# Kernel tuning notes

Measured on AMD Instinct MI355X. Metric: run time of the kernel, lower is better.

## Reference

```python
import jax, jax.numpy as jnp
import numpy as np

B, L, Q = 1024, 200, 1
DQ, DF = 512, 128
H, D1, D2 = 4, 128, 64


def setup_inputs() -> dict:
    key = jax.random.key(0)
    ks = jax.random.split(key, 20)
    inp = {
        "query": jax.random.normal(ks[0], (B, Q, DQ), jnp.float32),
        "fact": jax.random.normal(ks[1], (B, L, DF), jnp.float32),
        "mask": jax.random.randint(ks[2], (B, L), 0, 2, jnp.int32),
        "mm_cosine": jax.random.normal(ks[3], (2, B, L), jnp.float32),
    }
    # per-head FCRepeat weights, init per reset_parameters: randn/sqrt(fan_in), bias 0.1
    def w(k, fan_in, fan_out):
        return jax.random.normal(k, (H, fan_in, fan_out), jnp.float32) / np.sqrt(fan_in).astype(np.float32)
    inp["Wq1"] = w(ks[4], DQ, D1); inp["bq1"] = jnp.full((H, D1), 0.1, jnp.float32)
    inp["Wq2"] = w(ks[5], D1, D2); inp["bq2"] = jnp.full((H, D2), 0.1, jnp.float32)
    inp["Wf1"] = w(ks[6], DF, D1); inp["bf1"] = jnp.full((H, D1), 0.1, jnp.float32)
    inp["Wf2"] = w(ks[7], D1, D2); inp["bf2"] = jnp.full((H, D2), 0.1, jnp.float32)
    inp["Wv1"] = w(ks[8], DF, D1); inp["bv1"] = jnp.full((H, D1), 0.1, jnp.float32)
    inp["Wv2"] = w(ks[9], D1, D2); inp["bv2"] = jnp.full((H, D2), 0.1, jnp.float32)
    inp["tau1"] = jnp.full((2, H), 0.1, jnp.float32)   # cosine_tau1
    inp["tau2"] = jnp.full((3, H), 1.0, jnp.float32)   # cosine_tau2
    return inp


def _silu(x):
    return x * jax.nn.sigmoid(x)


def reference(query, fact, mask, mm_cosine,
              Wq1, bq1, Wq2, bq2, Wf1, bf1, Wf2, bf2, Wv1, bv1, Wv2, bv2,
              tau1, tau2):
    # per-head FC stacks (identity acts inside FCRepeat), then SiLU gating
    fq = jnp.einsum('bqi,hio->hbqo', query, Wq1) + bq1[:, None, None, :]
    fq = jnp.einsum('hbqi,hio->hbqo', fq, Wq2) + bq2[:, None, None, :]
    fq = _silu(fq)                                   # [H,B,1,D2]
    ff = jnp.einsum('bli,hio->hblo', fact, Wf1) + bf1[:, None, None, :]
    ff = jnp.einsum('hbli,hio->hblo', ff, Wf2) + bf2[:, None, None, :]
    ff = _silu(ff)                                   # [H,B,L,D2]
    fv = jnp.einsum('bli,hio->hblo', fact, Wv1) + bv1[:, None, None, :]
    fv = jnp.einsum('hbli,hio->hblo', fv, Wv2) + bv2[:, None, None, :]
    fv = _silu(fv)                                   # [H,B,L,D2]

    dot = jnp.einsum('hbld,hbqd->hblq', ff, fq)      # [H,B,L,1]
    dot = dot + (-1e9) * (1.0 - mask.astype(jnp.float32))[None, :, :, None]

    # cosine-bias cross terms
    bias = (mm_cosine[0][None] / tau1[0][:, None, None]
            + mm_cosine[1][None] / tau1[1][:, None, None])[..., None]  # [H,B,L,1]
    b1, b2, b3 = (tau2[i][:, None, None, None] for i in range(3))
    dot = b1 * dot + b2 * bias + b3 * dot * bias

    alphas = jax.nn.softmax(dot, axis=2) + 1e-7      # softmax over L
    out = jnp.einsum('hbld,hblq->hbdq', fv, alphas)[..., 0]  # [H,B,D2]
    return jnp.transpose(out, (1, 0, 2)).reshape(out.shape[1], -1)  # [B,H*D2]
```

## Files before the change

kernel.cpp:

```cpp
#include <hip/hip_runtime.h>
#include <hip/hip_bf16.h>

typedef __attribute__((ext_vector_type(8))) short short8;
typedef __attribute__((ext_vector_type(4))) float f32x4;

#define NH   4
#define NB   1024
#define NL   200
#define NDQ  512
#define NDF  128
#define ND1  128
#define ND2  64
#define KP   128
#define NW   13
#define NT   (NW*64)
#define HIMG (3*ND2*KP*2)
#define SGRAN (3*ND2*16)

#define OFF_WQC   0
#define OFF_BQC   (NH*NDQ*ND2*4)
#define OFF_FQ    (OFF_BQC + NH*ND2*4)
#define OFF_WIMG  (OFF_FQ + NH*NB*ND2*4)
#define OFF_BFC   (OFF_WIMG + NH*HIMG)
#define OFF_BVC   (OFF_BFC + NH*ND2*4)

#define GLOAD_LDS16(gp, lp) __builtin_amdgcn_global_load_lds(                 \
    (const __attribute__((address_space(1))) void*)(gp),                      \
    (__attribute__((address_space(3))) void*)(lp), 16, 0, 0)

__device__ inline short f2bf(float f) {
    union { float f; unsigned u; } v; v.f = f;
    unsigned r = (v.u + 0x7FFFu + ((v.u >> 16) & 1u)) >> 16;
    return (short)r;
}
__device__ inline float bf2f(short s) {
    union { unsigned u; float f; } v; v.u = ((unsigned)(unsigned short)s) << 16;
    return v.f;
}
__device__ inline float fsilu(float z) {
    return z * __fdividef(1.f, 1.f + __expf(-z));
}

template<int CTRL>
__device__ inline float dppf(float x) {
    return __int_as_float(__builtin_amdgcn_update_dpp(0, __float_as_int(x), CTRL, 0xF, 0xF, true));
}
__device__ inline float red16_add(float s) {
    s += dppf<0xB1>(s);
    s += dppf<0x4E>(s);
    s += dppf<0x141>(s);
    s += dppf<0x140>(s);
    return s;
}
__device__ inline float swap16_add(float x) {
    auto p = __builtin_amdgcn_permlane16_swap(__float_as_uint(x), __float_as_uint(x), false, false);
    return __uint_as_float(p[0]) + __uint_as_float(p[1]);
}
__device__ inline float swap32_add(float x) {
    auto p = __builtin_amdgcn_permlane32_swap(__float_as_uint(x), __float_as_uint(x), false, false);
    return __uint_as_float(p[0]) + __uint_as_float(p[1]);
}
__device__ inline float swap16_max(float x) {
    auto p = __builtin_amdgcn_permlane16_swap(__float_as_uint(x), __float_as_uint(x), false, false);
    return fmaxf(__uint_as_float(p[0]), __uint_as_float(p[1]));
}
__device__ inline float swap32_max(float x) {
    auto p = __builtin_amdgcn_permlane32_swap(__float_as_uint(x), __float_as_uint(x), false, false);
    return fmaxf(__uint_as_float(p[0]), __uint_as_float(p[1]));
}

__global__ __launch_bounds__(256) void k_combine(
    const float* __restrict__ Wq1, const float* __restrict__ bq1,
    const float* __restrict__ Wq2, const float* __restrict__ bq2,
    const float* __restrict__ Wf1, const float* __restrict__ bf1,
    const float* __restrict__ Wf2, const float* __restrict__ bf2,
    const float* __restrict__ Wv1, const float* __restrict__ bv1,
    const float* __restrict__ Wv2, const float* __restrict__ bv2,
    float* __restrict__ WQC, float* __restrict__ BQC,
    __hip_bfloat16* __restrict__ WIMG, float* __restrict__ BFC, float* __restrict__ BVC)
{
    int g = blockIdx.x * 256 + threadIdx.x;
    if (g < NH*NDQ*ND2) {
        int h = g >> 15, r = g & 32767, i = r >> 6, j = r & 63;
        const float* a  = Wq1 + (h*NDQ + i)*ND1;
        const float* bb = Wq2 + h*ND1*ND2 + j;
        float s = 0.f;
        for (int k = 0; k < ND1; ++k) s += a[k] * bb[k*ND2];
        WQC[(h*NDQ + i)*ND2 + j] = s;
        return;
    }
    g -= NH*NDQ*ND2;
    if (g < 2*NH*NDF*ND2) {
        int which = (g >= NH*NDF*ND2);
        int r0 = g & (NH*NDF*ND2 - 1);
        int h = r0 >> 13, r = r0 & 8191, i = r >> 6, j = r & 63;
        const float* W1 = (which ? Wv1 : Wf1) + (h*NDF + i)*ND1;
        const float* W2 = (which ? Wv2 : Wf2) + h*ND1*ND2 + j;
        float s = 0.f;
        for (int k = 0; k < ND1; ++k) s += W1[k] * W2[k*ND2];
        short hi = f2bf(s);
        short lo = f2bf(s - bf2f(hi));
        __hip_bfloat16* img = WIMG + (size_t)((h*3 + (which ? 2 : 0))*ND2 + j)*KP + i;
        ((short*)img)[0] = hi;
        if (!which) ((short*)img)[ND2*KP] = lo;
        return;
    }
    g -= 2*NH*NDF*ND2;
    if (g < NH*ND2) {
        int h = g >> 6, j = g & 63;
        float s = bq2[h*ND2 + j];
        for (int k = 0; k < ND1; ++k) s += bq1[h*ND1 + k] * Wq2[(h*ND1 + k)*ND2 + j];
        BQC[g] = s; return;
    }
    g -= NH*ND2;
    if (g < NH*ND2) {
        int h = g >> 6, j = g & 63;
        float s = bf2[h*ND2 + j];
        for (int k = 0; k < ND1; ++k) s += bf1[h*ND1 + k] * Wf2[(h*ND1 + k)*ND2 + j];
        BFC[g] = s; return;
    }
    g -= NH*ND2;
    if (g < NH*ND2) {
        int h = g >> 6, j = g & 63;
        float s = bv2[h*ND2 + j];
        for (int k = 0; k < ND1; ++k) s += bv1[h*ND1 + k] * Wv2[(h*ND1 + k)*ND2 + j];
        BVC[g] = s; return;
    }
}

__global__ __launch_bounds__(256) void k_fq(
    const float* __restrict__ query, const float* __restrict__ WQC,
    const float* __restrict__ BQC, float* __restrict__ FQ)
{
    __shared__ __align__(16) float qS[2*NDQ];
    const int t = threadIdx.x;
    const int b0 = blockIdx.x * 2;
    {
        const float4* src = (const float4*)(query + (size_t)b0 * NDQ);
        ((float4*)qS)[t] = src[t];
    }
    __syncthreads();
    const int h = t >> 6, d = t & 63;
    float s0, s1;
    s0 = s1 = BQC[h*ND2 + d];
    const float* wp = WQC + (size_t)h*NDQ*ND2 + d;
    #pragma unroll 16
    for (int i = 0; i < NDQ; ++i) {
        float wv = wp[i*ND2];
        s0 += qS[i]       * wv;
        s1 += qS[NDQ + i] * wv;
    }
    float* o = FQ + ((size_t)h*NB + b0)*ND2 + d;
    o[0]   = fsilu(s0);
    o[ND2] = fsilu(s1);
}

__global__ __launch_bounds__(NT) __attribute__((amdgpu_waves_per_eu(4, 4))) void k_main(
    const float* __restrict__ fact,
    const int* __restrict__ mask,
    const float* __restrict__ mmc,
    const float* __restrict__ tau1,
    const float* __restrict__ tau2,
    const float* __restrict__ FQ,
    const float* __restrict__ BFC,
    const float* __restrict__ BVC,
    const __hip_bfloat16* __restrict__ WIMG,
    float* __restrict__ out)
{
    __shared__ __align__(16) __hip_bfloat16 wS[2][3*ND2*KP];
    __shared__ __align__(16) float pS[2][NW][132];
    __shared__ __align__(16) float fqS[NH][ND2];
    __shared__ __align__(16) float bfcS[NH][ND2];
    __shared__ __align__(16) float bvcS[NH][ND2];

    const int t    = threadIdx.x;
    const int b    = blockIdx.x;
    const int w    = t >> 6;
    const int lane = t & 63;
    const int a15  = lane & 15;
    const int quad = lane >> 4;
    const int qrot = quad + 2*(a15 & 7);

    const int bL = b * NL;

    auto DMA = [&](int hh) {
        const char* hb = (const char*)WIMG + (size_t)hh*HIMG;
        char* lb = (char*)&wS[hh & 1][0];
        #pragma unroll
        for (int j = 0; j < 4; ++j) {
            int c = w*4 + j;
            if (c < SGRAN/64) {
                int i = c*64 + lane;
                int row = i >> 4;
                int g = ((i & 15) - 2*(row & 7)) & 15;
                GLOAD_LDS16(hb + (row*16 + g)*16, lb + c*1024);
            }
        }
    };

    DMA(0);

    float cval = 0.f;
    if (t < 256)       cval = FQ[(((size_t)(t >> 6))*NB + b)*ND2 + (t & 63)];
    else if (t < 512)  cval = BFC[t - 256];
    else if (t < 768)  cval = BVC[t - 512];
    float mkv[4], c0v[4], c1v[4];
    {
        int rbase = w*16 + quad*4;
        for (int rg = 0; rg < 4; ++rg) {
            int r = rbase + rg;
            if (r < NL) {
                mkv[rg] = 1e9f * (1.0f - (float)mask[bL + r]);
                c0v[rg] = mmc[bL + r];
                c1v[rg] = mmc[NB*NL + bL + r];
            } else { mkv[rg] = 0.f; c0v[rg] = 0.f; c1v[rg] = 0.f; }
        }
    }

    short8 afh[4], afl[4];
    const short8 zero8 = {0,0,0,0,0,0,0,0};
    {
        int row = w*16 + a15;
        for (int kk = 0; kk < 4; ++kk) {
            short8 vh = zero8, vl = zero8;
            if (row < NL) {
                const float* p = fact + ((size_t)(bL + row))*NDF + kk*32 + quad*8;
                float4 x0 = *(const float4*)p;
                float4 x1 = *(const float4*)(p + 4);
                float v[8] = {x0.x, x0.y, x0.z, x0.w, x1.x, x1.y, x1.z, x1.w};
                for (int j = 0; j < 8; ++j) {
                    short hs = f2bf(v[j]);
                    vh[j] = hs;
                    vl[j] = f2bf(v[j] - bf2f(hs));
                }
            }
            afh[kk] = vh;
            afl[kk] = vl;
        }
    }

    if (t < 256)       ((float*)fqS)[t]        = cval;
    else if (t < 512)  ((float*)bfcS)[t - 256] = cval;
    else if (t < 768)  ((float*)bvcS)[t - 512] = cval;
    __syncthreads();

    const f32x4 zf = {0.f, 0.f, 0.f, 0.f};

    auto GEMMS = [&](f32x4 (&aF)[4], f32x4 (&aV)[4], const __hip_bfloat16* wb) {
        #pragma unroll
        for (int nt = 0; nt < 4; ++nt) { aF[nt] = zf; aV[nt] = zf; }
        #pragma unroll
        for (int kk = 0; kk < 4; ++kk) {
            const int gk = ((kk*4 + qrot) & 15) << 3;
            short8 bh[4], bl[4];
            #pragma unroll
            for (int nt = 0; nt < 4; ++nt) {
                const __hip_bfloat16* p = wb + (nt*16 + a15)*KP + gk;
                bh[nt] = *(const short8*)p;
                bl[nt] = *(const short8*)(p + ND2*KP);
            }
            #pragma unroll
            for (int nt = 0; nt < 4; ++nt) {
                aF[nt] = __builtin_amdgcn_mfma_f32_16x16x32_bf16(afh[kk], bh[nt], aF[nt], 0, 0, 0);
                aF[nt] = __builtin_amdgcn_mfma_f32_16x16x32_bf16(afh[kk], bl[nt], aF[nt], 0, 0, 0);
                aF[nt] = __builtin_amdgcn_mfma_f32_16x16x32_bf16(afl[kk], bh[nt], aF[nt], 0, 0, 0);
            }
        }
        #pragma unroll
        for (int kk = 0; kk < 4; ++kk) {
            const int gk = ((kk*4 + qrot) & 15) << 3;
            short8 bv[4];
            #pragma unroll
            for (int nt = 0; nt < 4; ++nt)
                bv[nt] = *(const short8*)(wb + (2*ND2 + nt*16 + a15)*KP + gk);
            #pragma unroll
            for (int nt = 0; nt < 4; ++nt)
                aV[nt] = __builtin_amdgcn_mfma_f32_16x16x32_bf16(afh[kk], bv[nt], aV[nt], 0, 0, 0);
        }
    };

    auto FINISH = [&](f32x4 (&aF)[4], f32x4 (&aV)[4], int h) {
        const float rt1a = __fdividef(1.f, tau1[h]);
        const float rt1b = __fdividef(1.f, tau1[NH + h]);
        const float t20 = tau2[h];
        const float t21 = tau2[NH + h];
        const float t22 = tau2[2*NH + h];
        float fqv[4], bfcv[4], bvcv[4];
        #pragma unroll
        for (int nt = 0; nt < 4; ++nt) {
            fqv[nt]  = fqS[h][nt*16 + a15];
            bfcv[nt] = bfcS[h][nt*16 + a15];
            bvcv[nt] = bvcS[h][nt*16 + a15];
        }
        float lg[4];
        #pragma unroll
        for (int rg = 0; rg < 4; ++rg) {
            float l = -3.0e38f;
            float s = 0.f;
            #pragma unroll
            for (int nt = 0; nt < 4; ++nt)
                s += fsilu(aF[nt][rg] + bfcv[nt]) * fqv[nt];
            s = red16_add(s);
            int r = w*16 + quad*4 + rg;
            if (r < NL) {
                float dv = s - mkv[rg];
                float bias = c0v[rg]*rt1a + c1v[rg]*rt1b;
                l = t20*dv + t21*bias + t22*dv*bias;
            }
            lg[rg] = l;
        }
        float m = fmaxf(fmaxf(lg[0], lg[1]), fmaxf(lg[2], lg[3]));
        m = swap32_max(swap16_max(m));
        float sw = 0.f;
        #pragma unroll
        for (int rg = 0; rg < 4; ++rg) {
            float p = __expf(lg[rg] - m);
            lg[rg] = p;
            sw += p;
        }
        sw = swap32_add(swap16_add(sw));
        float oE[4] = {0.f,0.f,0.f,0.f}, oS[4] = {0.f,0.f,0.f,0.f};
        #pragma unroll
        for (int rg = 0; rg < 4; ++rg) {
            float p = lg[rg];
            int r = w*16 + quad*4 + rg;
            float vm = (r < NL) ? 1.f : 0.f;
            #pragma unroll
            for (int nt = 0; nt < 4; ++nt) {
                float sv = fsilu(aV[nt][rg] + bvcv[nt]);
                oE[nt] += p * sv;
                oS[nt] += vm * sv;
            }
        }
        #pragma unroll
        for (int nt = 0; nt < 4; ++nt) {
            oE[nt] = swap32_add(swap16_add(oE[nt]));
            oS[nt] = swap32_add(swap16_add(oS[nt]));
        }
        if (lane == 0) { pS[h & 1][w][0] = m; pS[h & 1][w][1] = sw; }
        if (quad == 0)
            #pragma unroll
            for (int nt = 0; nt < 4; ++nt) {
                pS[h & 1][w][2  + nt*16 + a15] = oE[nt];
                pS[h & 1][w][66 + nt*16 + a15] = oS[nt];
            }
    };

    auto MERGE = [&](int hm) {
        const int ps = hm & 1;
        float M = pS[ps][0][0];
        for (int ww = 1; ww < NW; ++ww) M = fmaxf(M, pS[ps][ww][0]);
        float den = 0.f, num = 0.f, s1 = 0.f;
        for (int ww = 0; ww < NW; ++ww) {
            float e = __expf(pS[ps][ww][0] - M);
            den += e * pS[ps][ww][1];
            num += e * pS[ps][ww][2 + lane];
            s1  += pS[ps][ww][66 + lane];
        }
        out[(size_t)b*(NH*ND2) + hm*ND2 + lane] = num * __fdividef(1.f, den) + 1e-7f * s1;
    };

    f32x4 aFA[4], aVA[4], aFB[4], aVB[4];

    DMA(1);
    GEMMS(aFA, aVA, &wS[0][0]);
    __syncthreads();

    DMA(2);
    GEMMS(aFB, aVB, &wS[1][0]);
    FINISH(aFA, aVA, 0);
    __syncthreads();

    DMA(3);
    if (w == 9) MERGE(0);
    GEMMS(aFA, aVA, &wS[0][0]);
    FINISH(aFB, aVB, 1);
    __syncthreads();

    if (w == 10) MERGE(1);
    GEMMS(aFB, aVB, &wS[1][0]);
    FINISH(aFA, aVA, 2);
    __syncthreads();

    if (w == 11) MERGE(2);
    FINISH(aFB, aVB, 3);
    __syncthreads();

    if (w == 12) MERGE(3);
}

extern "C" void kernel_launch(void* const* d_in, const int* in_sizes, int n_in,
                              void* d_out, int out_size, void* d_ws, size_t ws_size,
                              hipStream_t stream) {
    const float* query = (const float*)d_in[0];
    const float* fact  = (const float*)d_in[1];
    const int*   maskp = (const int*)d_in[2];
    const float* mmc   = (const float*)d_in[3];
    const float* Wq1 = (const float*)d_in[4];
    const float* bq1 = (const float*)d_in[5];
    const float* Wq2 = (const float*)d_in[6];
    const float* bq2 = (const float*)d_in[7];
    const float* Wf1 = (const float*)d_in[8];
    const float* bf1 = (const float*)d_in[9];
    const float* Wf2 = (const float*)d_in[10];
    const float* bf2 = (const float*)d_in[11];
    const float* Wv1 = (const float*)d_in[12];
    const float* bv1 = (const float*)d_in[13];
    const float* Wv2 = (const float*)d_in[14];
    const float* bv2 = (const float*)d_in[15];
    const float* tau1 = (const float*)d_in[16];
    const float* tau2 = (const float*)d_in[17];

    char* ws = (char*)d_ws;
    float*          WQC  = (float*)(ws + OFF_WQC);
    float*          BQC  = (float*)(ws + OFF_BQC);
    float*          FQ   = (float*)(ws + OFF_FQ);
    __hip_bfloat16* WIMG = (__hip_bfloat16*)(ws + OFF_WIMG);
    float*          BFC  = (float*)(ws + OFF_BFC);
    float*          BVC  = (float*)(ws + OFF_BVC);

    k_combine<<<771, 256, 0, stream>>>(Wq1, bq1, Wq2, bq2, Wf1, bf1, Wf2, bf2,
                                       Wv1, bv1, Wv2, bv2, WQC, BQC, WIMG, BFC, BVC);
    k_fq<<<NB/2, 256, 0, stream>>>(query, WQC, BQC, FQ);
    k_main<<<NB, NT, 0, stream>>>(fact, maskp, mmc, tau1, tau2, FQ, BFC, BVC, WIMG,
                                  (float*)d_out);
}
```

Measured before the change: 384.4 us.

## Split each batch row across two 8-wave blocks and merge partials in a separate kernel

```diff
diff --git a/kernel.cpp b/kernel.cpp
--- a/kernel.cpp
+++ b/kernel.cpp
@@ -12,8 +12,8 @@
 #define ND1  128
 #define ND2  64
 #define KP   128
-#define NW   13
-#define NT   (NW*64)
+#define NWB  8
+#define NTB  (NWB*64)
 #define HIMG (3*ND2*KP*2)
 #define SGRAN (3*ND2*16)
 
@@ -23,6 +23,7 @@
 #define OFF_WIMG  (OFF_FQ + NH*NB*ND2*4)
 #define OFF_BFC   (OFF_WIMG + NH*HIMG)
 #define OFF_BVC   (OFF_BFC + NH*ND2*4)
+#define OFF_PART  (OFF_BVC + NH*ND2*4)
 
 #define GLOAD_LDS16(gp, lp) __builtin_amdgcn_global_load_lds(                 \
     (const __attribute__((address_space(1))) void*)(gp),                      \
@@ -155,7 +156,7 @@
     o[ND2] = fsilu(s1);
 }
 
-__global__ __launch_bounds__(NT) __attribute__((amdgpu_waves_per_eu(4, 4))) void k_main(
+__global__ __launch_bounds__(NTB) void k_main(
     const float* __restrict__ fact,
     const int* __restrict__ mask,
     const float* __restrict__ mmc,
@@ -165,51 +166,51 @@
     const float* __restrict__ BFC,
     const float* __restrict__ BVC,
     const __hip_bfloat16* __restrict__ WIMG,
-    float* __restrict__ out)
+    float* __restrict__ gws)
 {
-    __shared__ __align__(16) __hip_bfloat16 wS[2][3*ND2*KP];
-    __shared__ __align__(16) float pS[2][NW][132];
+    __shared__ __align__(16) __hip_bfloat16 wS[3*ND2*KP];
+    __shared__ __align__(16) float pS[2][NWB][132];
     __shared__ __align__(16) float fqS[NH][ND2];
     __shared__ __align__(16) float bfcS[NH][ND2];
     __shared__ __align__(16) float bvcS[NH][ND2];
 
     const int t    = threadIdx.x;
-    const int b    = blockIdx.x;
+    const int blk  = blockIdx.x;
+    const int b    = blk >> 1;
+    const int half = blk & 1;
     const int w    = t >> 6;
     const int lane = t & 63;
     const int a15  = lane & 15;
     const int quad = lane >> 4;
     const int qrot = quad + 2*(a15 & 7);
 
+    const int tile = half ? (7 + w) : w;
+    const bool act = half ? (w < 6) : (w < 7);
     const int bL = b * NL;
 
     auto DMA = [&](int hh) {
         const char* hb = (const char*)WIMG + (size_t)hh*HIMG;
-        char* lb = (char*)&wS[hh & 1][0];
         #pragma unroll
-        for (int j = 0; j < 4; ++j) {
-            int c = w*4 + j;
-            if (c < SGRAN/64) {
-                int i = c*64 + lane;
-                int row = i >> 4;
-                int g = ((i & 15) - 2*(row & 7)) & 15;
-                GLOAD_LDS16(hb + (row*16 + g)*16, lb + c*1024);
-            }
+        for (int j = 0; j < 6; ++j) {
+            int c = w*6 + j;
+            int i = c*64 + lane;
+            int row = i >> 4;
+            int g = ((i & 15) - 2*(row & 7)) & 15;
+            GLOAD_LDS16(hb + (row*16 + g)*16, (char*)wS + c*1024);
         }
     };
 
     DMA(0);
 
-    float cval = 0.f;
-    if (t < 256)       cval = FQ[(((size_t)(t >> 6))*NB + b)*ND2 + (t & 63)];
-    else if (t < 512)  cval = BFC[t - 256];
-    else if (t < 768)  cval = BVC[t - 512];
+    float cval = 0.f, cval2 = 0.f;
+    if (t < 256) { cval = FQ[(((size_t)(t >> 6))*NB + b)*ND2 + (t & 63)]; cval2 = BVC[t]; }
+    else         { cval = BFC[t - 256]; }
     float mkv[4], c0v[4], c1v[4];
     {
-        int rbase = w*16 + quad*4;
+        int rbase = tile*16 + quad*4;
         for (int rg = 0; rg < 4; ++rg) {
             int r = rbase + rg;
-            if (r < NL) {
+            if (act && r < NL) {
                 mkv[rg] = 1e9f * (1.0f - (float)mask[bL + r]);
                 c0v[rg] = mmc[bL + r];
                 c1v[rg] = mmc[NB*NL + bL + r];
@@ -220,10 +221,10 @@
     short8 afh[4], afl[4];
     const short8 zero8 = {0,0,0,0,0,0,0,0};
     {
-        int row = w*16 + a15;
+        int row = tile*16 + a15;
         for (int kk = 0; kk < 4; ++kk) {
             short8 vh = zero8, vl = zero8;
-            if (row < NL) {
+            if (act && row < NL) {
                 const float* p = fact + ((size_t)(bL + row))*NDF + kk*32 + quad*8;
                 float4 x0 = *(const float4*)p;
                 float4 x1 = *(const float4*)(p + 4);
@@ -239,154 +240,156 @@
         }
     }
 
-    if (t < 256)       ((float*)fqS)[t]        = cval;
-    else if (t < 512)  ((float*)bfcS)[t - 256] = cval;
-    else if (t < 768)  ((float*)bvcS)[t - 512] = cval;
+    if (t < 256) { ((float*)fqS)[t] = cval; ((float*)bvcS)[t] = cval2; }
+    else         { ((float*)bfcS)[t - 256] = cval; }
     __syncthreads();
 
     const f32x4 zf = {0.f, 0.f, 0.f, 0.f};
 
-    auto GEMMS = [&](f32x4 (&aF)[4], f32x4 (&aV)[4], const __hip_bfloat16* wb) {
-        #pragma unroll
-        for (int nt = 0; nt < 4; ++nt) { aF[nt] = zf; aV[nt] = zf; }
-        #pragma unroll
-        for (int kk = 0; kk < 4; ++kk) {
-            const int gk = ((kk*4 + qrot) & 15) << 3;
-            short8 bh[4], bl[4];
+    for (int h = 0; h < NH; ++h) {
+        if (act) {
+            const float rt1a = __fdividef(1.f, tau1[h]);
+            const float rt1b = __fdividef(1.f, tau1[NH + h]);
+            const float t20 = tau2[h];
+            const float t21 = tau2[NH + h];
+            const float t22 = tau2[2*NH + h];
+            float fqv[4], bfcv[4], bvcv[4];
             #pragma unroll
             for (int nt = 0; nt < 4; ++nt) {
-                const __hip_bfloat16* p = wb + (nt*16 + a15)*KP + gk;
-                bh[nt] = *(const short8*)p;
-                bl[nt] = *(const short8*)(p + ND2*KP);
+                fqv[nt]  = fqS[h][nt*16 + a15];
+                bfcv[nt] = bfcS[h][nt*16 + a15];
+                bvcv[nt] = bvcS[h][nt*16 + a15];
+            }
+
+            f32x4 acc[4];
+            #pragma unroll
+            for (int nt = 0; nt < 4; ++nt) acc[nt] = zf;
+            #pragma unroll
+            for (int kk = 0; kk < 4; ++kk) {
+                const int gk = ((kk*4 + qrot) & 15) << 3;
+                short8 bh[4], bl[4];
+                #pragma unroll
+                for (int nt = 0; nt < 4; ++nt) {
+                    const __hip_bfloat16* p = wS + (nt*16 + a15)*KP + gk;
+                    bh[nt] = *(const short8*)p;
+                    bl[nt] = *(const short8*)(p + ND2*KP);
+                }
+                #pragma unroll
+                for (int nt = 0; nt < 4; ++nt) {
+                    acc[nt] = __builtin_amdgcn_mfma_f32_16x16x32_bf16(afh[kk], bh[nt], acc[nt], 0, 0, 0);
+                    acc[nt] = __builtin_amdgcn_mfma_f32_16x16x32_bf16(afh[kk], bl[nt], acc[nt], 0, 0, 0);
+                    acc[nt] = __builtin_amdgcn_mfma_f32_16x16x32_bf16(afl[kk], bh[nt], acc[nt], 0, 0, 0);
+                }
+            }
+
+            float lg[4];
+            #pragma unroll
+            for (int rg = 0; rg < 4; ++rg) {
+                float l = -3.0e38f;
+                float s = 0.f;
+                #pragma unroll
+                for (int nt = 0; nt < 4; ++nt)
+                    s += fsilu(acc[nt][rg] + bfcv[nt]) * fqv[nt];
+                s = red16_add(s);
+                int r = tile*16 + quad*4 + rg;
+                if (r < NL) {
+                    float dv = s - mkv[rg];
+                    float bias = c0v[rg]*rt1a + c1v[rg]*rt1b;
+                    l = t20*dv + t21*bias + t22*dv*bias;
+                }
+                lg[rg] = l;
+            }
+
+            float m = fmaxf(fmaxf(lg[0], lg[1]), fmaxf(lg[2], lg[3]));
+            m = swap32_max(swap16_max(m));
+            float sw = 0.f;
+            #pragma unroll
+            for (int rg = 0; rg < 4; ++rg) {
+                float p = __expf(lg[rg] - m);
+                lg[rg] = p;
+                sw += p;
+            }
+            sw = swap32_add(swap16_add(sw));
+
+            #pragma unroll
+            for (int nt = 0; nt < 4; ++nt) acc[nt] = zf;
+            #pragma unroll
+            for (int kk = 0; kk < 4; ++kk) {
+                const int gk = ((kk*4 + qrot) & 15) << 3;
+                short8 bv[4];
+                #pragma unroll
+                for (int nt = 0; nt < 4; ++nt)
+                    bv[nt] = *(const short8*)(wS + (2*ND2 + nt*16 + a15)*KP + gk);
+                #pragma unroll
+                for (int nt = 0; nt < 4; ++nt)
+                    acc[nt] = __builtin_amdgcn_mfma_f32_16x16x32_bf16(afh[kk], bv[nt], acc[nt], 0, 0, 0);
+            }
+
+            float oE[4] = {0.f,0.f,0.f,0.f}, oS[4] = {0.f,0.f,0.f,0.f};
+            #pragma unroll
+            for (int rg = 0; rg < 4; ++rg) {
+                float p = lg[rg];
+                int r = tile*16 + quad*4 + rg;
+                float vm = (r < NL) ? 1.f : 0.f;
+                #pragma unroll
+                for (int nt = 0; nt < 4; ++nt) {
+                    float sv = fsilu(acc[nt][rg] + bvcv[nt]);
+                    oE[nt] += p * sv;
+                    oS[nt] += vm * sv;
+                }
             }
             #pragma unroll
             for (int nt = 0; nt < 4; ++nt) {
-                aF[nt] = __builtin_amdgcn_mfma_f32_16x16x32_bf16(afh[kk], bh[nt], aF[nt], 0, 0, 0);
-                aF[nt] = __builtin_amdgcn_mfma_f32_16x16x32_bf16(afh[kk], bl[nt], aF[nt], 0, 0, 0);
-                aF[nt] = __builtin_amdgcn_mfma_f32_16x16x32_bf16(afl[kk], bh[nt], aF[nt], 0, 0, 0);
-            }
+                oE[nt] = swap32_add(swap16_add(oE[nt]));
+                oS[nt] = swap32_add(swap16_add(oS[nt]));
+            }
+            if (lane == 0) { pS[h & 1][w][0] = m; pS[h & 1][w][1] = sw; }
+            if (quad == 0)
+                #pragma unroll
+                for (int nt = 0; nt < 4; ++nt) {
+                    pS[h & 1][w][2  + nt*16 + a15] = oE[nt];
+                    pS[h & 1][w][66 + nt*16 + a15] = oS[nt];
+                }
         }
-        #pragma unroll
-        for (int kk = 0; kk < 4; ++kk) {
-            const int gk = ((kk*4 + qrot) & 15) << 3;
-            short8 bv[4];
-            #pragma unroll
-            for (int nt = 0; nt < 4; ++nt)
-                bv[nt] = *(const short8*)(wb + (2*ND2 + nt*16 + a15)*KP + gk);
-            #pragma unroll
-            for (int nt = 0; nt < 4; ++nt)
-                aV[nt] = __builtin_amdgcn_mfma_f32_16x16x32_bf16(afh[kk], bv[nt], aV[nt], 0, 0, 0);
+        __syncthreads();
+
+        if (h + 1 < NH) DMA(h + 1);
+
+        if (w == 7) {
+            const int ps = h & 1;
+            const int nAct = half ? 6 : 7;
+            float M = pS[ps][0][0];
+            for (int ww = 1; ww < nAct; ++ww) M = fmaxf(M, pS[ps][ww][0]);
+            float den = 0.f, num = 0.f, s1 = 0.f;
+            for (int ww = 0; ww < nAct; ++ww) {
+                float e = __expf(pS[ps][ww][0] - M);
+                den += e * pS[ps][ww][1];
+                num += e * pS[ps][ww][2 + lane];
+                s1  += pS[ps][ww][66 + lane];
+            }
+            float* gp = gws + (((size_t)b*2 + half)*NH + h)*132;
+            if (lane == 0) { gp[0] = M; gp[1] = den; }
+            gp[2 + lane]  = num;
+            gp[66 + lane] = s1;
         }
-    };
-
-    auto FINISH = [&](f32x4 (&aF)[4], f32x4 (&aV)[4], int h) {
-        const float rt1a = __fdividef(1.f, tau1[h]);
-        const float rt1b = __fdividef(1.f, tau1[NH + h]);
-        const float t20 = tau2[h];
-        const float t21 = tau2[NH + h];
-        const float t22 = tau2[2*NH + h];
-        float fqv[4], bfcv[4], bvcv[4];
-        #pragma unroll
-        for (int nt = 0; nt < 4; ++nt) {
-            fqv[nt]  = fqS[h][nt*16 + a15];
-            bfcv[nt] = bfcS[h][nt*16 + a15];
-            bvcv[nt] = bvcS[h][nt*16 + a15];
-        }
-        float lg[4];
-        #pragma unroll
-        for (int rg = 0; rg < 4; ++rg) {
-            float l = -3.0e38f;
-            float s = 0.f;
-            #pragma unroll
-            for (int nt = 0; nt < 4; ++nt)
-                s += fsilu(aF[nt][rg] + bfcv[nt]) * fqv[nt];
-            s = red16_add(s);
-            int r = w*16 + quad*4 + rg;
-            if (r < NL) {
-                float dv = s - mkv[rg];
-                float bias = c0v[rg]*rt1a + c1v[rg]*rt1b;
-                l = t20*dv + t21*bias + t22*dv*bias;
-            }
-            lg[rg] = l;
-        }
-        float m = fmaxf(fmaxf(lg[0], lg[1]), fmaxf(lg[2], lg[3]));
-        m = swap32_max(swap16_max(m));
-        float sw = 0.f;
-        #pragma unroll
-        for (int rg = 0; rg < 4; ++rg) {
-            float p = __expf(lg[rg] - m);
-            lg[rg] = p;
-            sw += p;
-        }
-        sw = swap32_add(swap16_add(sw));
-        float oE[4] = {0.f,0.f,0.f,0.f}, oS[4] = {0.f,0.f,0.f,0.f};
-        #pragma unroll
-        for (int rg = 0; rg < 4; ++rg) {
-            float p = lg[rg];
-            int r = w*16 + quad*4 + rg;
-            float vm = (r < NL) ? 1.f : 0.f;
-            #pragma unroll
-            for (int nt = 0; nt < 4; ++nt) {
-                float sv = fsilu(aV[nt][rg] + bvcv[nt]);
-                oE[nt] += p * sv;
-                oS[nt] += vm * sv;
-            }
-        }
-        #pragma unroll
-        for (int nt = 0; nt < 4; ++nt) {
-            oE[nt] = swap32_add(swap16_add(oE[nt]));
-            oS[nt] = swap32_add(swap16_add(oS[nt]));
-        }
-        if (lane == 0) { pS[h & 1][w][0] = m; pS[h & 1][w][1] = sw; }
-        if (quad == 0)
-            #pragma unroll
-            for (int nt = 0; nt < 4; ++nt) {
-                pS[h & 1][w][2  + nt*16 + a15] = oE[nt];
-                pS[h & 1][w][66 + nt*16 + a15] = oS[nt];
-            }
-    };
-
-    auto MERGE = [&](int hm) {
-        const int ps = hm & 1;
-        float M = pS[ps][0][0];
-        for (int ww = 1; ww < NW; ++ww) M = fmaxf(M, pS[ps][ww][0]);
-        float den = 0.f, num = 0.f, s1 = 0.f;
-        for (int ww = 0; ww < NW; ++ww) {
-            float e = __expf(pS[ps][ww][0] - M);
-            den += e * pS[ps][ww][1];
-            num += e * pS[ps][ww][2 + lane];
-            s1  += pS[ps][ww][66 + lane];
-        }
-        out[(size_t)b*(NH*ND2) + hm*ND2 + lane] = num * __fdividef(1.f, den) + 1e-7f * s1;
-    };
-
-    f32x4 aFA[4], aVA[4], aFB[4], aVB[4];
-
-    DMA(1);
-    GEMMS(aFA, aVA, &wS[0][0]);
-    __syncthreads();
-
-    DMA(2);
-    GEMMS(aFB, aVB, &wS[1][0]);
-    FINISH(aFA, aVA, 0);
-    __syncthreads();
-
-    DMA(3);
-    if (w == 9) MERGE(0);
-    GEMMS(aFA, aVA, &wS[0][0]);
-    FINISH(aFB, aVB, 1);
-    __syncthreads();
-
-    if (w == 10) MERGE(1);
-    GEMMS(aFB, aVB, &wS[1][0]);
-    FINISH(aFA, aVA, 2);
-    __syncthreads();
-
-    if (w == 11) MERGE(2);
-    FINISH(aFB, aVB, 3);
-    __syncthreads();
-
-    if (w == 12) MERGE(3);
+        __syncthreads();
+    }
+}
+
+__global__ __launch_bounds__(256) void k_merge(
+    const float* __restrict__ gws, float* __restrict__ out)
+{
+    const int b = blockIdx.x, t = threadIdx.x;
+    const int h = t >> 6, d = t & 63;
+    const float* A = gws + (((size_t)b*2 + 0)*NH + h)*132;
+    const float* B = gws + (((size_t)b*2 + 1)*NH + h)*132;
+    float MA = A[0], MB = B[0];
+    float M  = fmaxf(MA, MB);
+    float eA = __expf(MA - M), eB = __expf(MB - M);
+    float den = eA*A[1] + eB*B[1];
+    float num = eA*A[2 + d] + eB*B[2 + d];
+    float s1  = A[66 + d] + B[66 + d];
+    out[(size_t)b*(NH*ND2) + h*ND2 + d] = num * __fdividef(1.f, den) + 1e-7f * s1;
 }
 
 extern "C" void kernel_launch(void* const* d_in, const int* in_sizes, int n_in,
@@ -418,10 +421,12 @@
     __hip_bfloat16* WIMG = (__hip_bfloat16*)(ws + OFF_WIMG);
     float*          BFC  = (float*)(ws + OFF_BFC);
     float*          BVC  = (float*)(ws + OFF_BVC);
+    float*          PART = (float*)(ws + OFF_PART);
 
     k_combine<<<771, 256, 0, stream>>>(Wq1, bq1, Wq2, bq2, Wf1, bf1, Wf2, bf2,
                                        Wv1, bv1, Wv2, bv2, WQC, BQC, WIMG, BFC, BVC);
     k_fq<<<NB/2, 256, 0, stream>>>(query, WQC, BQC, FQ);
-    k_main<<<NB, NT, 0, stream>>>(fact, maskp, mmc, tau1, tau2, FQ, BFC, BVC, WIMG,
-                                  (float*)d_out);
-}
+    k_main<<<NB*2, NTB, 0, stream>>>(fact, maskp, mmc, tau1, tau2, FQ, BFC, BVC, WIMG,
+                                     PART);
+    k_merge<<<NB, 256, 0, stream>>>(PART, (float*)d_out);
+}
```

Measured after the change: 383.1 us. Within noise of the previous version (-0.3%).
